# Performance work log

Hardware: AMD Instinct MI355X
Metric: run time of the kernel (lower is better)

Reference implementation:

```python
import jax, jax.numpy as jnp
import numpy as np


def _deform_conv2d(x, offset, weight, stride=(1, 1), pad=(1, 1), dilation=(1, 1)):
    # x: [B,C,H,W]; offset: [B, 2*Goff*kh*kw, oh, ow]; weight: [OC, C//Gw, kh, kw]
    B, C, H, W = x.shape
    OC, Cg, kh, kw = weight.shape
    Gw = C // Cg
    K = kh * kw
    sh, sw = stride
    ph, pw = pad
    dh, dw = dilation
    oh = (H + 2 * ph - (dh * (kh - 1) + 1)) // sh + 1
    ow = (W + 2 * pw - (dw * (kw - 1) + 1)) // sw + 1
    Goff = offset.shape[1] // (2 * K)
    # torchvision layout: per offset group, per kernel tap k, (dy, dx)
    off = offset.reshape(B, Goff, K, 2, oh, ow)
    ki = jnp.arange(K) // kw  # kernel row per tap
    kj = jnp.arange(K) % kw   # kernel col per tap
    base_y = jnp.arange(oh) * sh - ph
    base_x = jnp.arange(ow) * sw - pw
    gy = (base_y[None, :] + (ki * dh)[:, None]).astype(x.dtype)  # [K, oh]
    gx = (base_x[None, :] + (kj * dw)[:, None]).astype(x.dtype)  # [K, ow]
    py = off[:, :, :, 0] + gy[None, None, :, :, None]  # [B,Goff,K,oh,ow]
    px = off[:, :, :, 1] + gx[None, None, :, None, :]
    cpg = C // Goff  # channels per offset group
    py = jnp.repeat(py, cpg, axis=1)  # [B,C,K,oh,ow]
    px = jnp.repeat(px, cpg, axis=1)
    xf = x.reshape(B, C, H * W)
    y0 = jnp.floor(py)
    x0 = jnp.floor(px)
    ty = py - y0
    tx = px - x0
    y0i = y0.astype(jnp.int32)
    x0i = x0.astype(jnp.int32)

    def gather(cy, cx):
        valid = (cy >= 0) & (cy < H) & (cx >= 0) & (cx < W)
        idx = jnp.clip(cy, 0, H - 1) * W + jnp.clip(cx, 0, W - 1)
        v = jnp.take_along_axis(xf, idx.reshape(B, C, -1), axis=2).reshape(idx.shape)
        return jnp.where(valid, v, jnp.zeros((), x.dtype))

    # bilinear sample, zero padding outside image (matches torchvision)
    v = (gather(y0i, x0i) * (1 - ty) * (1 - tx)
         + gather(y0i, x0i + 1) * (1 - ty) * tx
         + gather(y0i + 1, x0i) * ty * (1 - tx)
         + gather(y0i + 1, x0i + 1) * ty * tx)  # [B,C,K,oh,ow]
    v = v.reshape(B, Gw, Cg, K, oh, ow)
    wg = weight.reshape(Gw, OC // Gw, Cg, K)
    out = jnp.einsum('bgckhw,gock->bgohw', v, wg)
    return out.reshape(B, OC, oh, ow)


def setup_inputs() -> dict:
    key = jax.random.key(0)
    k1, k2, k3 = jax.random.split(key, 3)
    x = jax.random.normal(k1, (8, 64, 56, 56), dtype=jnp.float32)
    offset = jax.random.normal(k2, (8, 18, 56, 56), dtype=jnp.float32)
    weight = jax.random.normal(k3, (64, 64, 3, 3), dtype=jnp.float32) * 0.05
    return {"input": x, "offset": offset, "weight": weight}


def reference(input, offset, weight):
    return _deform_conv2d(input, offset, weight, stride=(1, 1), pad=(1, 1), dilation=(1, 1))
```

## Files before the change

### kernel.cpp

```cpp
#include <hip/hip_runtime.h>
#include <hip/hip_fp16.h>


typedef _Float16 f16x8 __attribute__((ext_vector_type(8)));
typedef float    f32x4 __attribute__((ext_vector_type(4)));

namespace {
constexpr int Bn = 8, Cn = 64, Hn = 56, Wn = 56;
constexpr int Kk = 9, OCn = 64;
constexpr int NPIX = 56 * 56;
constexpr int CK   = Cn * Kk;
constexpr int TP   = 32;
constexpr int TILES = NPIX / TP;
constexpr int XTILES = NPIX / 64;
constexpr int KSTEPS = CK / 32;
}

__device__ __forceinline__ __half2 u2h(unsigned u) {
    union { unsigned u; __half2 h; } x; x.u = u; return x.h;
}
__device__ __forceinline__ unsigned bcast_h(float f) {
    unsigned short hs = __half_as_ushort(__float2half(f));
    return (unsigned)hs * 0x10001u;
}

__global__ __launch_bounds__(256) void prep_kernel(
    const float* __restrict__ x, const float* __restrict__ w,
    unsigned short* __restrict__ xh, unsigned short* __restrict__ wh2)
{
    const int tid = threadIdx.x;
    if (blockIdx.x >= 392) {
        const int i = (blockIdx.x - 392) * 256 + tid;
        if (i < OCn * CK) {
            const int j    = i & 7;
            const int lane = (i >> 3) & 63;
            const int rest = i >> 9;
            const int og   = rest / KSTEPS;
            const int oc   = og * 16 + (lane & 15);
            const int kglob = (rest % KSTEPS) * 32 + (lane >> 4) * 8 + j;
            const int tap = kglob >> 6;
            const int c   = kglob & 63;
            wh2[i] = __half_as_ushort(__float2half(w[oc * CK + c * Kk + tap]));
        }
        return;
    }
    __shared__ unsigned short lds[64][66];
    const int b  = blockIdx.x / XTILES;
    const int t0 = (blockIdx.x % XTILES) * 64;
    const float* xb = x + (size_t)b * Cn * NPIX;
    {
        const int hw0 = (tid & 15) * 4;
        #pragma unroll
        for (int i = 0; i < 4; ++i) {
            const int c = (tid >> 4) + i * 16;
            const float4 v = *(const float4*)(xb + (size_t)c * NPIX + t0 + hw0);
            lds[hw0 + 0][c] = __half_as_ushort(__float2half(v.x));
            lds[hw0 + 1][c] = __half_as_ushort(__float2half(v.y));
            lds[hw0 + 2][c] = __half_as_ushort(__float2half(v.z));
            lds[hw0 + 3][c] = __half_as_ushort(__float2half(v.w));
        }
    }
    __syncthreads();
    {
        const int co = (tid & 7) * 8;
        #pragma unroll
        for (int i = 0; i < 2; ++i) {
            const int hw = (tid >> 3) + i * 32;
            unsigned short tmp[8] __attribute__((aligned(16)));
            #pragma unroll
            for (int j = 0; j < 8; ++j) tmp[j] = lds[hw][co + j];
            *(uint4*)(xh + ((size_t)b * NPIX + t0 + hw) * Cn + co) = *(const uint4*)tmp;
        }
    }
}

__global__ __launch_bounds__(256, 4) void deform_fused(
    const unsigned short* __restrict__ xh, const float* __restrict__ off,
    const unsigned short* __restrict__ wh2, float* __restrict__ out)
{
    __shared__ uint4 smpw[Kk * TP];
    __shared__ int4  smpa[Kk * TP];
    __shared__ __align__(16) uint4 vbuf[2][24 * TP];

    const int tid = threadIdx.x;
    const int b  = blockIdx.x / TILES;
    const int p0 = (blockIdx.x % TILES) * TP;
    const unsigned short* xb = xh + (size_t)b * NPIX * Cn;
    const float* offb = off + (size_t)b * 18 * NPIX;

    for (int e = tid; e < Kk * TP; e += 256) {
        const int k  = e >> 5;
        const int px = e & 31;
        const int p  = p0 + px;
        const int oy = p / Wn, ox = p % Wn;
        const int ki = k / 3, kj = k % 3;
        const float offy = offb[(size_t)(2 * k)     * NPIX + p];
        const float offx = offb[(size_t)(2 * k + 1) * NPIX + p];
        const float py  = offy + (float)(oy - 1 + ki);
        const float pxv = offx + (float)(ox - 1 + kj);
        const float y0f = floorf(py), x0f = floorf(pxv);
        const float ty = py - y0f, tx = pxv - x0f;
        const int y0 = (int)y0f, x0 = (int)x0f;
        const int y1 = y0 + 1, x1 = x0 + 1;
        const bool vy0 = (y0 >= 0) & (y0 < Hn);
        const bool vy1 = (y1 >= 0) & (y1 < Hn);
        const bool vx0 = (x0 >= 0) & (x0 < Wn);
        const bool vx1 = (x1 >= 0) & (x1 < Wn);
        const int cy0 = min(max(y0, 0), Hn - 1);
        const int cy1 = min(max(y1, 0), Hn - 1);
        const int cx0 = min(max(x0, 0), Wn - 1);
        const int cx1 = min(max(x1, 0), Wn - 1);
        uint4 wq;
        wq.x = bcast_h((vy0 && vx0) ? (1.f - ty) * (1.f - tx) : 0.f);
        wq.y = bcast_h((vy0 && vx1) ? (1.f - ty) * tx         : 0.f);
        wq.z = bcast_h((vy1 && vx0) ? ty * (1.f - tx)         : 0.f);
        wq.w = bcast_h((vy1 && vx1) ? ty * tx                 : 0.f);
        int4 av;
        av.x = (cy0 * Wn + cx0) * Cn;
        av.y = (cy0 * Wn + cx1) * Cn;
        av.z = (cy1 * Wn + cx0) * Cn;
        av.w = (cy1 * Wn + cx1) * Cn;
        smpw[e] = wq;
        smpa[e] = av;
    }
    __syncthreads();

    uint4 s0[3], s1[3], s2[3], s3[3], wqr[3];
    int vidx[3];

    auto stage = [&](int chunk) {
        #pragma unroll
        for (int j = 0; j < 3; ++j) {
            const int u    = tid + 256 * j;
            const int oct  = u & 7;
            const int px   = (u >> 3) & 31;
            const int kloc = u >> 8;
            const int m    = (chunk * 3 + kloc) * TP + px;
            const int4 av  = smpa[m];
            wqr[j] = smpw[m];
            const int co = oct * 8;
            s0[j] = *(const uint4*)(xb + av.x + co);
            s1[j] = *(const uint4*)(xb + av.y + co);
            s2[j] = *(const uint4*)(xb + av.z + co);
            s3[j] = *(const uint4*)(xb + av.w + co);
            vidx[j] = (kloc * 8 + oct) * TP + px;
        }
    };
    auto blend = [&](int buf) {
        #pragma unroll
        for (int j = 0; j < 3; ++j) {
            const __half2 w00 = u2h(wqr[j].x), w01 = u2h(wqr[j].y);
            const __half2 w10 = u2h(wqr[j].z), w11 = u2h(wqr[j].w);
            uint4 res;
            unsigned* rp = (unsigned*)&res;
            #pragma unroll
            for (int q = 0; q < 4; ++q) {
                __half2 a = __hmul2(w00, u2h(((const unsigned*)&s0[j])[q]));
                a = __hfma2(w01, u2h(((const unsigned*)&s1[j])[q]), a);
                a = __hfma2(w10, u2h(((const unsigned*)&s2[j])[q]), a);
                a = __hfma2(w11, u2h(((const unsigned*)&s3[j])[q]), a);
                rp[q] = *(const unsigned*)&a;
            }
            vbuf[buf][vidx[j]] = res;
        }
    };

    const int lane = tid & 63;
    const int og   = tid >> 6;
    const int hi   = lane >> 4;
    const int lr   = lane & 15;
    const uint4* ab = (const uint4*)wh2 + (size_t)og * KSTEPS * 64 + lane;
    f32x4 acc0 = {0.f, 0.f, 0.f, 0.f};
    f32x4 acc1 = {0.f, 0.f, 0.f, 0.f};

    auto mfma_chunk = [&](int chunk, int buf) {
        #pragma unroll
        for (int kl = 0; kl < 6; ++kl) {
            union { uint4 u; f16x8 h; } a, b0, b1;
            a.u  = ab[(chunk * 6 + kl) * 64];
            b0.u = vbuf[buf][(kl * 4 + hi) * TP + lr];
            b1.u = vbuf[buf][(kl * 4 + hi) * TP + 16 + lr];
            acc0 = __builtin_amdgcn_mfma_f32_16x16x32_f16(a.h, b0.h, acc0, 0, 0, 0);
            acc1 = __builtin_amdgcn_mfma_f32_16x16x32_f16(a.h, b1.h, acc1, 0, 0, 0);
        }
    };

    stage(0);
    blend(0);
    __syncthreads();
    stage(1);
    mfma_chunk(0, 0);
    blend(1);
    __syncthreads();
    stage(2);
    mfma_chunk(1, 1);
    blend(0);
    __syncthreads();
    mfma_chunk(2, 0);

    float* ob = out + ((size_t)b * OCn + og * 16 + hi * 4) * NPIX + p0 + lr;
    #pragma unroll
    for (int r = 0; r < 4; ++r) {
        ob[(size_t)r * NPIX]      = acc0[r];
        ob[(size_t)r * NPIX + 16] = acc1[r];
    }
}

extern "C" void kernel_launch(void* const* d_in, const int* in_sizes, int n_in,
                              void* d_out, int out_size, void* d_ws, size_t ws_size,
                              hipStream_t stream) {
    const float* x   = (const float*)d_in[0];
    const float* off = (const float*)d_in[1];
    const float* w   = (const float*)d_in[2];
    float* out = (float*)d_out;
    unsigned short* wh2 = (unsigned short*)d_ws;
    unsigned short* xh  = (unsigned short*)((char*)d_ws + 131072);

    hipLaunchKernelGGL(prep_kernel, dim3(392 + 144), dim3(256), 0, stream, x, w, xh, wh2);
    hipLaunchKernelGGL(deform_fused, dim3(Bn * TILES), dim3(256), 0, stream,
                       xh, off, wh2, out);
}
```

Baseline: 22.06 us.

## Pipeline deformable gather per tap with triple-buffered LDS and register prefetch

Reorganizes the main loop from three 3-tap chunks into nine per-tap steps. Bilinear gathers are prefetched three taps ahead in registers, and the blended fp16 tile goes into a triple-buffered LDS array. The weight fragments for the next tap are also loaded into registers ahead of the MFMAs. The aim is to hide global gather latency behind the MFMA work. The cost is nine block barriers instead of three, plus higher register pressure from keeping several taps in flight.

New measurement: 21.96 us. About the same (-0.4%).

```diff
diff --git a/kernel.cpp b/kernel.cpp
--- a/kernel.cpp
+++ b/kernel.cpp
@@ -80,7 +80,7 @@
 {
     __shared__ uint4 smpw[Kk * TP];
     __shared__ int4  smpa[Kk * TP];
-    __shared__ __align__(16) uint4 vbuf[2][24 * TP];
+    __shared__ __align__(16) uint4 vbuf[3][8 * TP];
 
     const int tid = threadIdx.x;
     const int b  = blockIdx.x / TILES;
@@ -125,78 +125,79 @@
     }
     __syncthreads();
 
-    uint4 s0[3], s1[3], s2[3], s3[3], wqr[3];
-    int vidx[3];
-
-    auto stage = [&](int chunk) {
-        #pragma unroll
-        for (int j = 0; j < 3; ++j) {
-            const int u    = tid + 256 * j;
-            const int oct  = u & 7;
-            const int px   = (u >> 3) & 31;
-            const int kloc = u >> 8;
-            const int m    = (chunk * 3 + kloc) * TP + px;
-            const int4 av  = smpa[m];
-            wqr[j] = smpw[m];
-            const int co = oct * 8;
-            s0[j] = *(const uint4*)(xb + av.x + co);
-            s1[j] = *(const uint4*)(xb + av.y + co);
-            s2[j] = *(const uint4*)(xb + av.z + co);
-            s3[j] = *(const uint4*)(xb + av.w + co);
-            vidx[j] = (kloc * 8 + oct) * TP + px;
-        }
-    };
-    auto blend = [&](int buf) {
-        #pragma unroll
-        for (int j = 0; j < 3; ++j) {
-            const __half2 w00 = u2h(wqr[j].x), w01 = u2h(wqr[j].y);
-            const __half2 w10 = u2h(wqr[j].z), w11 = u2h(wqr[j].w);
-            uint4 res;
-            unsigned* rp = (unsigned*)&res;
-            #pragma unroll
-            for (int q = 0; q < 4; ++q) {
-                __half2 a = __hmul2(w00, u2h(((const unsigned*)&s0[j])[q]));
-                a = __hfma2(w01, u2h(((const unsigned*)&s1[j])[q]), a);
-                a = __hfma2(w10, u2h(((const unsigned*)&s2[j])[q]), a);
-                a = __hfma2(w11, u2h(((const unsigned*)&s3[j])[q]), a);
-                rp[q] = *(const unsigned*)&a;
-            }
-            vbuf[buf][vidx[j]] = res;
-        }
-    };
+    const int oct = tid & 7;
+    const int gpx = (tid >> 3) & 31;
+    const int co  = oct * 8;
 
     const int lane = tid & 63;
     const int og   = tid >> 6;
     const int hi   = lane >> 4;
     const int lr   = lane & 15;
     const uint4* ab = (const uint4*)wh2 + (size_t)og * KSTEPS * 64 + lane;
+
+    uint4 s0[3], s1[3], s2[3], s3[3], wqr[3];
+    uint4 aF[2][2];
     f32x4 acc0 = {0.f, 0.f, 0.f, 0.f};
     f32x4 acc1 = {0.f, 0.f, 0.f, 0.f};
 
-    auto mfma_chunk = [&](int chunk, int buf) {
-        #pragma unroll
-        for (int kl = 0; kl < 6; ++kl) {
+    auto stage = [&](int k) {
+        const int sl = k % 3;
+        const int m  = k * TP + gpx;
+        const int4 av = smpa[m];
+        wqr[sl] = smpw[m];
+        s0[sl] = *(const uint4*)(xb + av.x + co);
+        s1[sl] = *(const uint4*)(xb + av.y + co);
+        s2[sl] = *(const uint4*)(xb + av.z + co);
+        s3[sl] = *(const uint4*)(xb + av.w + co);
+    };
+    auto loadA = [&](int k) {
+        const int sl = k & 1;
+        aF[sl][0] = ab[(k * 2 + 0) * 64];
+        aF[sl][1] = ab[(k * 2 + 1) * 64];
+    };
+    auto blend = [&](int k) {
+        const int sl = k % 3;
+        const __half2 w00 = u2h(wqr[sl].x), w01 = u2h(wqr[sl].y);
+        const __half2 w10 = u2h(wqr[sl].z), w11 = u2h(wqr[sl].w);
+        uint4 res;
+        unsigned* rp = (unsigned*)&res;
+        #pragma unroll
+        for (int q = 0; q < 4; ++q) {
+            __half2 a = __hmul2(w00, u2h(((const unsigned*)&s0[sl])[q]));
+            a = __hfma2(w01, u2h(((const unsigned*)&s1[sl])[q]), a);
+            a = __hfma2(w10, u2h(((const unsigned*)&s2[sl])[q]), a);
+            a = __hfma2(w11, u2h(((const unsigned*)&s3[sl])[q]), a);
+            rp[q] = *(const unsigned*)&a;
+        }
+        vbuf[sl][oct * TP + gpx] = res;
+    };
+    auto mfma = [&](int k) {
+        const int sl = k % 3;
+        #pragma unroll
+        for (int kl = 0; kl < 2; ++kl) {
+            const int octr = kl * 4 + hi;
             union { uint4 u; f16x8 h; } a, b0, b1;
-            a.u  = ab[(chunk * 6 + kl) * 64];
-            b0.u = vbuf[buf][(kl * 4 + hi) * TP + lr];
-            b1.u = vbuf[buf][(kl * 4 + hi) * TP + 16 + lr];
+            a.u  = aF[k & 1][kl];
+            b0.u = vbuf[sl][octr * TP + lr];
+            b1.u = vbuf[sl][octr * TP + 16 + lr];
             acc0 = __builtin_amdgcn_mfma_f32_16x16x32_f16(a.h, b0.h, acc0, 0, 0, 0);
             acc1 = __builtin_amdgcn_mfma_f32_16x16x32_f16(a.h, b1.h, acc1, 0, 0, 0);
         }
     };
 
-    stage(0);
+    stage(0); stage(1); stage(2);
+    loadA(0);
     blend(0);
     __syncthreads();
-    stage(1);
-    mfma_chunk(0, 0);
-    blend(1);
-    __syncthreads();
-    stage(2);
-    mfma_chunk(1, 1);
-    blend(0);
-    __syncthreads();
-    mfma_chunk(2, 0);
+
+    #pragma unroll
+    for (int k = 0; k < Kk; ++k) {
+        if (k < Kk - 3) stage(k + 3);
+        if (k < Kk - 1) loadA(k + 1);
+        if (k < Kk - 1) blend(k + 1);
+        mfma(k);
+        __syncthreads();
+    }
 
     float* ob = out + ((size_t)b * OCn + og * 16 + hi * 4) * NPIX + p0 + lr;
     #pragma unroll
```
